# Optimization experiments

Hardware: AMD Instinct MI355X
Metric: run time of the kernel (lower is better)

## Reference

```python
import jax, jax.numpy as jnp
import numpy as np

ALPHA = 1.0          # gating temperature (train_alpha=False)
DEPTH = 4            # floor(log2(leaves=16))
LEAF_NUM = 16        # 2**DEPTH
N_INTERNAL = LEAF_NUM - 2  # nodes 1..14 (root handled separately)
B, D, OUT = 8192, 512, 64


def _prob(x, pw, aW, ab):
    # vectorized Node.prob with set_comps=True (comparators recomputed from batch mean)
    comp = -jnp.mean(x * pw, axis=0)                      # [in]
    dist = jax.nn.sigmoid(ALPHA * (pw * x + comp))        # [B, in]
    attn = jax.nn.softmax(x @ aW.T + ab, axis=-1)         # [B, in]
    return jnp.sum(dist * attn, axis=1, keepdims=True)    # [B, 1]


def setup_inputs() -> dict:
    key = jax.random.key(0)
    ks = jax.random.split(key, 12)
    s = 0.02
    return {
        "x": jax.random.normal(ks[0], (B, D), jnp.float32),
        # root node (input_size=D, output_size=D)
        "calc_W0": jax.random.normal(ks[1], (D, D), jnp.float32) * s,
        "calc_b0": jnp.zeros((D,), jnp.float32),
        "prob_w0": jax.random.uniform(ks[2], (D,), jnp.float32),
        "attn_W0": jax.random.normal(ks[3], (D, D), jnp.float32) * s,
        "attn_b0": jnp.zeros((D,), jnp.float32),
        # internal nodes 1..14 (input_size=2D, output_size=D), stacked
        "calc_W": jax.random.normal(ks[4], (N_INTERNAL, D, 2 * D), jnp.float32) * s,
        "calc_b": jnp.zeros((N_INTERNAL, D), jnp.float32),
        "prob_w": jax.random.uniform(ks[5], (N_INTERNAL, 2 * D), jnp.float32),
        "attn_W": jax.random.normal(ks[6], (N_INTERNAL, 2 * D, 2 * D), jnp.float32) * s,
        "attn_b": jnp.zeros((N_INTERNAL, 2 * D), jnp.float32),
        # leaf nodes: learned output vectors (torch.rand init)
        "leaf_out": jax.random.uniform(ks[7], (LEAF_NUM, OUT), jnp.float32),
    }


def reference(x, calc_W0, calc_b0, prob_w0, attn_W0, attn_b0,
              calc_W, calc_b, prob_w, attn_W, attn_b, leaf_out):
    outs, probab = {}, {}
    # root
    outs[0] = jax.nn.relu(x @ calc_W0.T + calc_b0)            # [B, D]
    p = _prob(x, prob_w0, attn_W0, attn_b0)                   # [B, 1]
    probab[1] = 1.0 - p
    probab[2] = p
    # internal nodes 1..leaf_num-2 (binary-tree routing)
    for n in range(1, LEAF_NUM - 1):
        parent = (n - 1) // 2
        inp = jnp.concatenate([outs[parent], x], axis=1)      # [B, 2D]
        outs[n] = jax.nn.relu(inp @ calc_W[n - 1].T + calc_b[n - 1])
        p = _prob(inp, prob_w[n - 1], attn_W[n - 1], attn_b[n - 1])
        probab[2 * n + 1] = probab[n] * (1.0 - p)
        probab[2 * n + 2] = probab[n] * p
    # leaves: indices LEAF_NUM-1 .. 2*LEAF_NUM-2
    leaf_p = jnp.concatenate([probab[i + LEAF_NUM - 1] for i in range(LEAF_NUM)], axis=1)  # [B, 16]
    # sum over leaves of probab * leaf_out == leaf_p @ leaf_out
    actions = leaf_p @ leaf_out                                # [B, OUT]
    return jax.nn.softmax(actions, axis=-1)
```

## Files before the change

kernel.cpp:

```cpp
#include <hip/hip_runtime.h>
#include <hip/hip_bf16.h>
#include <cstdint>


#define NROWS 8192
#define HALFD 512

typedef __bf16 bf16x8 __attribute__((ext_vector_type(8)));
typedef short  short8 __attribute__((ext_vector_type(8)));
typedef float  f32x4  __attribute__((ext_vector_type(4)));

union FragU { short8 s; bf16x8 b; };

struct GArgs {
  const __hip_bfloat16* A0[4];
  const __hip_bfloat16* Bw[4];
  const float* bias[4];
  const float* pw[4];
  const float* cm0[4];
  __hip_bfloat16* outB[4];
  float* csOut[4];
  float* S1[4];
  float* S2[4];
  int mode[4];
  int gx[4];
  int K[4];
};

__device__ __forceinline__ void gl2lds16(const void* g, void* l) {
  __builtin_amdgcn_global_load_lds((__attribute__((address_space(1))) void*)g,
                                   (__attribute__((address_space(3))) void*)l,
                                   16, 0, 0);
}

struct CvtArgs { const float* src[5]; __hip_bfloat16* dst[5]; int nblk[5]; };
__global__ void k_cvt(CvtArgs a) {
  int b = blockIdx.x, r = 0;
  while (b >= a.nblk[r]) { b -= a.nblk[r]; ++r; }
  const int i = (b * 256 + threadIdx.x) * 4;
  float4 v = *(const float4*)(a.src[r] + i);
  union { short4 s4; __hip_bfloat16 h[4]; } u;
  u.h[0] = __float2bfloat16(v.x);
  u.h[1] = __float2bfloat16(v.y);
  u.h[2] = __float2bfloat16(v.z);
  u.h[3] = __float2bfloat16(v.w);
  *(short4*)(a.dst[r] + i) = u.s4;
}

__global__ void k_colsum_f32(const float* __restrict__ src, float* __restrict__ dst) {
  int c  = blockIdx.x * 256 + threadIdx.x;
  int r0 = blockIdx.y * 256;
  float s = 0.f;
  for (int r = 0; r < 256; ++r) s += src[(size_t)(r0 + r) * HALFD + c];
  atomicAdd(&dst[c], s);
}

__global__ __launch_bounds__(256, 2)
void k_gemm(GArgs ga, const __hip_bfloat16* __restrict__ A1,
            const float* __restrict__ cm1) {
  __shared__ alignas(16) short As[128 * 64];
  __shared__ alignas(16) short Bs[128 * 64];

  const int z = blockIdx.z;
  const int id  = blockIdx.x + gridDim.x * blockIdx.y;
  const int xcd = id & 7;
  const int q   = id >> 3;
  const int bx  = q >> 3;
  const int by  = xcd * 8 + (q & 7);
  if (bx >= ga.gx[z]) return;

  const __hip_bfloat16* __restrict__ Ah0 = ga.A0[z];
  const __hip_bfloat16* __restrict__ Bw  = ga.Bw[z];
  const float* __restrict__ bias = ga.bias[z];
  const int K = ga.K[z];

  const int tid  = threadIdx.x;
  const int lane = tid & 63;
  const int wv   = tid >> 6;
  const int wm   = wv >> 1, wn = wv & 1;
  const int lr   = lane & 15, lg = lane >> 4;
  const int row0 = by * 128;
  const int col0 = bx * 128;

  f32x4 acc[4][4];
#pragma unroll
  for (int i = 0; i < 4; ++i)
#pragma unroll
    for (int j = 0; j < 4; ++j)
#pragma unroll
      for (int e = 0; e < 4; ++e) acc[i][j][e] = 0.f;

  const int sr = tid >> 3;
  const int sc = (((tid & 7) ^ (sr & 7)) << 3);
  const int sw = lr & 7;

  for (int kt = 0; kt < K; kt += 64) {
    const __hip_bfloat16* Asrc = (kt < HALFD) ? Ah0 : A1;
    const int kl = kt & (HALFD - 1);
    __syncthreads();
#pragma unroll
    for (int rnd = 0; rnd < 4; ++rnd) {
      const int r = rnd * 32 + sr;
      gl2lds16(Asrc + (size_t)(row0 + r) * HALFD + kl + sc,
               (char*)As + rnd * 4096 + wv * 1024);
      gl2lds16(Bw + (size_t)(col0 + r) * K + kt + sc,
               (char*)Bs + rnd * 4096 + wv * 1024);
    }
    __syncthreads();
#pragma unroll
    for (int kk = 0; kk < 64; kk += 32) {
      FragU a[4], b[4];
#pragma unroll
      for (int mi = 0; mi < 4; ++mi)
        a[mi].s = *(const short8*)(As + (wm * 64 + mi * 16 + lr) * 64 +
                                   ((((kk >> 3) + lg) ^ sw) << 3));
#pragma unroll
      for (int ni = 0; ni < 4; ++ni)
        b[ni].s = *(const short8*)(Bs + (wn * 64 + ni * 16 + lr) * 64 +
                                   ((((kk >> 3) + lg) ^ sw) << 3));
#pragma unroll
      for (int mi = 0; mi < 4; ++mi)
#pragma unroll
        for (int ni = 0; ni < 4; ++ni)
          acc[mi][ni] = __builtin_amdgcn_mfma_f32_16x16x32_bf16(a[mi].b, b[ni].b,
                                                               acc[mi][ni], 0, 0, 0);
    }
  }

  if (ga.mode[z] == 0) {
    __hip_bfloat16* outB = ga.outB[z];
    float* csOut = ga.csOut[z];
#pragma unroll
    for (int ni = 0; ni < 4; ++ni) {
      const int col  = col0 + wn * 64 + ni * 16 + lr;
      const float bv = bias[col];
      __hip_bfloat16* op = outB + (size_t)(col >> 9) * ((size_t)NROWS * HALFD) + (col & 511);
      float csum = 0.f;
#pragma unroll
      for (int mi = 0; mi < 4; ++mi) {
#pragma unroll
        for (int rg = 0; rg < 4; ++rg) {
          const int row = row0 + wm * 64 + mi * 16 + lg * 4 + rg;
          float v = acc[mi][ni][rg] + bv;
          v = v > 0.f ? v : 0.f;
          csum += v;
          op[(size_t)row * HALFD] = __float2bfloat16(v);
        }
      }
      csum += __shfl_xor(csum, 16);
      csum += __shfl_xor(csum, 32);
      if (lg == 0) atomicAdd(&csOut[col], csum);
    }
  } else {
    const float* __restrict__ pw  = ga.pw[z];
    const float* __restrict__ cm0 = ga.cm0[z];
    const int node  = col0 >> 10;
    const int slice = ((bx & 7) << 1) | wn;
    float* s1p = ga.S1[z] + (size_t)(node * 16 + slice) * NROWS;
    float* s2p = ga.S2[z] + (size_t)(node * 16 + slice) * NROWS;
    float bv[4], pwv[4], cmv[4];
    const __hip_bfloat16* Ain[4];
#pragma unroll
    for (int ni = 0; ni < 4; ++ni) {
      const int col = col0 + wn * 64 + ni * 16 + lr;
      bv[ni]  = bias[col];
      pwv[ni] = pw[col];
      const int ii   = col & 1023;
      const int half = ii >> 9;
      const int cc   = ii & 511;
      cmv[ni] = (half ? cm1[cc] : cm0[cc]) * (1.f / 8192.f);
      Ain[ni] = (half ? A1 : Ah0) + cc;
    }
#pragma unroll
    for (int mi = 0; mi < 4; ++mi) {
#pragma unroll
      for (int rg = 0; rg < 4; ++rg) {
        const int row = row0 + wm * 64 + mi * 16 + lg * 4 + rg;
        float s1 = 0.f, s2 = 0.f;
#pragma unroll
        for (int ni = 0; ni < 4; ++ni) {
          const float l = acc[mi][ni][rg] + bv[ni];
          const float e = __expf(l);
          const float inpv = __bfloat162float(Ain[ni][(size_t)row * HALFD]);
          const float zz = pwv[ni] * (inpv - cmv[ni]);
          const float dist = 1.f / (1.f + __expf(-zz));
          s1 += e;
          s2 += dist * e;
        }
#pragma unroll
        for (int off = 1; off < 16; off <<= 1) {
          s1 += __shfl_xor(s1, off);
          s2 += __shfl_xor(s2, off);
        }
        if (lr == 0) {
          s1p[row] = s1;
          s2p[row] = s2;
        }
      }
    }
  }
}

__global__ void k_finalize(const float* __restrict__ S1, const float* __restrict__ S2,
                           const float* __restrict__ leaf_out, float* __restrict__ out) {
  const int r    = (blockIdx.x * 256 + threadIdx.x) >> 6;
  const int lane = threadIdx.x & 63;
  float pb[31];
  pb[0] = 1.f;
#pragma unroll
  for (int n = 0; n < 15; ++n) {
    float a1 = 0.f, a2 = 0.f;
#pragma unroll
    for (int s = 0; s < 16; ++s) {
      a1 += S1[((size_t)n * 16 + s) * NROWS + r];
      a2 += S2[((size_t)n * 16 + s) * NROWS + r];
    }
    const float p = a2 / a1;
    pb[2 * n + 1] = pb[n] * (1.f - p);
    pb[2 * n + 2] = pb[n] * p;
  }
  float a = 0.f;
#pragma unroll
  for (int i = 0; i < 16; ++i) a += pb[15 + i] * leaf_out[i * 64 + lane];
  float m = a;
#pragma unroll
  for (int off = 1; off < 64; off <<= 1) m = fmaxf(m, __shfl_xor(m, off));
  const float e = __expf(a - m);
  float s = e;
#pragma unroll
  for (int off = 1; off < 64; off <<= 1) s += __shfl_xor(s, off);
  out[(size_t)r * 64 + lane] = e / s;
}

static constexpr size_t O_S1   = 0;
static constexpr size_t O_S2   = O_S1 + (size_t)15 * 16 * NROWS * 4;
static constexpr size_t O_XSUM = O_S2 + (size_t)15 * 16 * NROWS * 4;
static constexpr size_t O_CS   = O_XSUM + 512 * 4;
static constexpr size_t O_ZEND = O_CS + 7 * 512 * 4;
static constexpr size_t O_XB   = O_ZEND;
static constexpr size_t O_OUTS = O_XB + (size_t)NROWS * HALFD * 2;
static constexpr size_t O_CW0  = O_OUTS + 7 * (size_t)NROWS * HALFD * 2;
static constexpr size_t O_AW0  = O_CW0 + (size_t)512 * 512 * 2;
static constexpr size_t O_CW   = O_AW0 + (size_t)512 * 512 * 2;
static constexpr size_t O_AW   = O_CW + (size_t)14 * 512 * 1024 * 2;

extern "C" void kernel_launch(void* const* d_in, const int* in_sizes, int n_in,
                              void* d_out, int out_size, void* d_ws, size_t ws_size,
                              hipStream_t stream) {
  const float* x        = (const float*)d_in[0];
  const float* calc_b0  = (const float*)d_in[2];
  const float* prob_w0  = (const float*)d_in[3];
  const float* attn_b0  = (const float*)d_in[5];
  const float* calc_b   = (const float*)d_in[7];
  const float* prob_w   = (const float*)d_in[8];
  const float* attn_b   = (const float*)d_in[10];
  const float* leaf_out = (const float*)d_in[11];
  float* out = (float*)d_out;
  char* ws = (char*)d_ws;

  float* S1   = (float*)(ws + O_S1);
  float* S2   = (float*)(ws + O_S2);
  float* xsum = (float*)(ws + O_XSUM);
  float* cs   = (float*)(ws + O_CS);
  __hip_bfloat16* xb   = (__hip_bfloat16*)(ws + O_XB);
  __hip_bfloat16* outs = (__hip_bfloat16*)(ws + O_OUTS);
  __hip_bfloat16* cW0b = (__hip_bfloat16*)(ws + O_CW0);
  __hip_bfloat16* aW0b = (__hip_bfloat16*)(ws + O_AW0);
  __hip_bfloat16* cWb  = (__hip_bfloat16*)(ws + O_CW);
  __hip_bfloat16* aWb  = (__hip_bfloat16*)(ws + O_AW);
  const size_t OSZ = (size_t)NROWS * HALFD;
  const size_t NSL = (size_t)16 * NROWS;

  hipMemsetAsync(d_ws, 0, O_ZEND, stream);

  {
    CvtArgs ca{};
    ca.src[0] = x;                     ca.dst[0] = xb;   ca.nblk[0] = NROWS * HALFD / 1024;
    ca.src[1] = (const float*)d_in[1]; ca.dst[1] = cW0b; ca.nblk[1] = 512 * 512 / 1024;
    ca.src[2] = (const float*)d_in[4]; ca.dst[2] = aW0b; ca.nblk[2] = 512 * 512 / 1024;
    ca.src[3] = (const float*)d_in[6]; ca.dst[3] = cWb;  ca.nblk[3] = 14 * 512 * 1024 / 1024;
    ca.src[4] = (const float*)d_in[9]; ca.dst[4] = aWb;  ca.nblk[4] = 14 * 1024 * 1024 / 1024;
    int tot = ca.nblk[0] + ca.nblk[1] + ca.nblk[2] + ca.nblk[3] + ca.nblk[4];
    k_cvt<<<tot, 256, 0, stream>>>(ca);
  }
  k_colsum_f32<<<dim3(2, 32), 256, 0, stream>>>(x, xsum);

  {
    GArgs ga{};
    ga.mode[0] = 0; ga.gx[0] = 4; ga.K[0] = 512;
    ga.A0[0] = xb; ga.Bw[0] = cW0b; ga.bias[0] = calc_b0;
    ga.outB[0] = outs; ga.csOut[0] = cs;
    ga.mode[1] = 1; ga.gx[1] = 4; ga.K[1] = 512;
    ga.A0[1] = xb; ga.Bw[1] = aW0b; ga.bias[1] = attn_b0;
    ga.pw[1] = prob_w0; ga.cm0[1] = xsum;
    ga.S1[1] = S1; ga.S2[1] = S2;
    k_gemm<<<dim3(4, 64, 2), 256, 0, stream>>>(ga, xb, xsum);
  }
  {
    GArgs ga{};
    ga.mode[0] = 0; ga.gx[0] = 8; ga.K[0] = 1024;
    ga.A0[0] = outs; ga.Bw[0] = cWb; ga.bias[0] = calc_b;
    ga.outB[0] = outs + OSZ; ga.csOut[0] = cs + 512;
    ga.mode[1] = 1; ga.gx[1] = 16; ga.K[1] = 1024;
    ga.A0[1] = outs; ga.Bw[1] = aWb; ga.bias[1] = attn_b;
    ga.pw[1] = prob_w; ga.cm0[1] = cs;
    ga.S1[1] = S1 + (size_t)1 * NSL; ga.S2[1] = S2 + (size_t)1 * NSL;
    k_gemm<<<dim3(16, 64, 2), 256, 0, stream>>>(ga, xb, xsum);
  }
  {
    GArgs ga{};
    for (int i = 0; i < 2; ++i) {
      ga.mode[i] = 0; ga.gx[i] = 8; ga.K[i] = 1024;
      ga.A0[i] = outs + (size_t)(1 + i) * OSZ;
      ga.Bw[i] = cWb + (size_t)(2 + 2 * i) * 512 * 1024;
      ga.bias[i] = calc_b + (2 + 2 * i) * 512;
      ga.outB[i] = outs + (size_t)(3 + 2 * i) * OSZ;
      ga.csOut[i] = cs + (size_t)(3 + 2 * i) * 512;
    }
    for (int i = 0; i < 2; ++i) {
      const int zi = 2 + i;
      ga.mode[zi] = 1; ga.gx[zi] = 16; ga.K[zi] = 1024;
      ga.A0[zi] = outs + (size_t)(1 + i) * OSZ;
      ga.Bw[zi] = aWb + (size_t)(2 + 2 * i) * 1024 * 1024;
      ga.bias[zi] = attn_b + (2 + 2 * i) * 1024;
      ga.pw[zi] = prob_w + (2 + 2 * i) * 1024;
      ga.cm0[zi] = cs + (size_t)(1 + i) * 512;
      ga.S1[zi] = S1 + (size_t)(3 + 2 * i) * NSL;
      ga.S2[zi] = S2 + (size_t)(3 + 2 * i) * NSL;
    }
    k_gemm<<<dim3(16, 64, 4), 256, 0, stream>>>(ga, xb, xsum);
  }
  {
    GArgs ga{};
    for (int i = 0; i < 4; ++i) {
      ga.mode[i] = 1; ga.gx[i] = 16; ga.K[i] = 1024;
      ga.A0[i] = outs + (size_t)(3 + i) * OSZ;
      ga.Bw[i] = aWb + (size_t)(6 + 2 * i) * 1024 * 1024;
      ga.bias[i] = attn_b + (6 + 2 * i) * 1024;
      ga.pw[i] = prob_w + (6 + 2 * i) * 1024;
      ga.cm0[i] = cs + (size_t)(3 + i) * 512;
      ga.S1[i] = S1 + (size_t)(7 + 2 * i) * NSL;
      ga.S2[i] = S2 + (size_t)(7 + 2 * i) * NSL;
    }
    k_gemm<<<dim3(16, 64, 4), 256, 0, stream>>>(ga, xb, xsum);
  }

  k_finalize<<<NROWS * 64 / 256, 256, 0, stream>>>(S1, S2, leaf_out, out);
}
```

Baseline: 636.2 us.

## Use 256x256 GEMM tiles with 512 threads and double-buffered LDS prefetch

The GEMM kernel moves from 128x128 tiles with 4 waves to 256x256 tiles with 8 waves, and each wave now covers 128x64 outputs with twice the accumulators. LDS is double-buffered so the next K slab is loaded while the current one is multiplied, leaving one barrier per iteration instead of two. This aims to raise data reuse per byte loaded and hide global-to-LDS latency. In exchange it uses 128KB of LDS per block and more registers, which may cut occupancy, and the grid shrinks to fewer, larger blocks, which may leave CUs idle.

Measured after the change: 668.8 us. +5.1%, slower.

```diff
diff --git a/kernel.cpp b/kernel.cpp
--- a/kernel.cpp
+++ b/kernel.cpp
@@ -55,18 +55,18 @@
   atomicAdd(&dst[c], s);
 }
 
-__global__ __launch_bounds__(256, 2)
+__global__ __launch_bounds__(512, 2)
 void k_gemm(GArgs ga, const __hip_bfloat16* __restrict__ A1,
             const float* __restrict__ cm1) {
-  __shared__ alignas(16) short As[128 * 64];
-  __shared__ alignas(16) short Bs[128 * 64];
+  __shared__ alignas(16) short As[2][256 * 64];
+  __shared__ alignas(16) short Bs[2][256 * 64];
 
   const int z = blockIdx.z;
   const int id  = blockIdx.x + gridDim.x * blockIdx.y;
   const int xcd = id & 7;
   const int q   = id >> 3;
-  const int bx  = q >> 3;
-  const int by  = xcd * 8 + (q & 7);
+  const int bx  = q >> 2;
+  const int by  = xcd * 4 + (q & 3);
   if (bx >= ga.gx[z]) return;
 
   const __hip_bfloat16* __restrict__ Ah0 = ga.A0[z];
@@ -77,54 +77,69 @@
   const int tid  = threadIdx.x;
   const int lane = tid & 63;
   const int wv   = tid >> 6;
-  const int wm   = wv >> 1, wn = wv & 1;
+  const int wm   = wv >> 2, wn = wv & 3;
   const int lr   = lane & 15, lg = lane >> 4;
-  const int row0 = by * 128;
-  const int col0 = bx * 128;
-
-  f32x4 acc[4][4];
-#pragma unroll
-  for (int i = 0; i < 4; ++i)
+  const int sw   = lr & 7;
+  const int row0 = by * 256;
+  const int col0 = bx * 256;
+
+  f32x4 acc[8][4];
+#pragma unroll
+  for (int i = 0; i < 8; ++i)
 #pragma unroll
     for (int j = 0; j < 4; ++j)
 #pragma unroll
       for (int e = 0; e < 4; ++e) acc[i][j][e] = 0.f;
 
-  const int sr = tid >> 3;
-  const int sc = (((tid & 7) ^ (sr & 7)) << 3);
-  const int sw = lr & 7;
-
+  const int sr  = tid >> 3;
+  const int sc  = (((tid & 7) ^ (sr & 7)) << 3);
+  const int wvB = wv * 1024;
+
+#pragma unroll
+  for (int rnd = 0; rnd < 4; ++rnd) {
+    const int r = rnd * 64 + sr;
+    gl2lds16(Ah0 + (size_t)(row0 + r) * HALFD + sc, (char*)As[0] + rnd * 8192 + wvB);
+    gl2lds16(Bw  + (size_t)(col0 + r) * K + sc,     (char*)Bs[0] + rnd * 8192 + wvB);
+  }
+  __syncthreads();
+
+  int cur = 0;
   for (int kt = 0; kt < K; kt += 64) {
-    const __hip_bfloat16* Asrc = (kt < HALFD) ? Ah0 : A1;
-    const int kl = kt & (HALFD - 1);
-    __syncthreads();
-#pragma unroll
-    for (int rnd = 0; rnd < 4; ++rnd) {
-      const int r = rnd * 32 + sr;
-      gl2lds16(Asrc + (size_t)(row0 + r) * HALFD + kl + sc,
-               (char*)As + rnd * 4096 + wv * 1024);
-      gl2lds16(Bw + (size_t)(col0 + r) * K + kt + sc,
-               (char*)Bs + rnd * 4096 + wv * 1024);
-    }
-    __syncthreads();
+    const int kn = kt + 64;
+    if (kn < K) {
+      const __hip_bfloat16* Asrc = (kn < HALFD) ? Ah0 : A1;
+      const int kl = kn & (HALFD - 1);
+#pragma unroll
+      for (int rnd = 0; rnd < 4; ++rnd) {
+        const int r = rnd * 64 + sr;
+        gl2lds16(Asrc + (size_t)(row0 + r) * HALFD + kl + sc,
+                 (char*)As[cur ^ 1] + rnd * 8192 + wvB);
+        gl2lds16(Bw + (size_t)(col0 + r) * K + kn + sc,
+                 (char*)Bs[cur ^ 1] + rnd * 8192 + wvB);
+      }
+    }
+    const short* Ab = As[cur];
+    const short* Bb = Bs[cur];
 #pragma unroll
     for (int kk = 0; kk < 64; kk += 32) {
-      FragU a[4], b[4];
-#pragma unroll
-      for (int mi = 0; mi < 4; ++mi)
-        a[mi].s = *(const short8*)(As + (wm * 64 + mi * 16 + lr) * 64 +
+      FragU a[8], b[4];
+#pragma unroll
+      for (int mi = 0; mi < 8; ++mi)
+        a[mi].s = *(const short8*)(Ab + (wm * 128 + mi * 16 + lr) * 64 +
                                    ((((kk >> 3) + lg) ^ sw) << 3));
 #pragma unroll
       for (int ni = 0; ni < 4; ++ni)
-        b[ni].s = *(const short8*)(Bs + (wn * 64 + ni * 16 + lr) * 64 +
+        b[ni].s = *(const short8*)(Bb + (wn * 64 + ni * 16 + lr) * 64 +
                                    ((((kk >> 3) + lg) ^ sw) << 3));
 #pragma unroll
-      for (int mi = 0; mi < 4; ++mi)
+      for (int mi = 0; mi < 8; ++mi)
 #pragma unroll
         for (int ni = 0; ni < 4; ++ni)
           acc[mi][ni] = __builtin_amdgcn_mfma_f32_16x16x32_bf16(a[mi].b, b[ni].b,
                                                                acc[mi][ni], 0, 0, 0);
     }
+    __syncthreads();
+    cur ^= 1;
   }
 
   if (ga.mode[z] == 0) {
@@ -137,10 +152,10 @@
       __hip_bfloat16* op = outB + (size_t)(col >> 9) * ((size_t)NROWS * HALFD) + (col & 511);
       float csum = 0.f;
 #pragma unroll
-      for (int mi = 0; mi < 4; ++mi) {
+      for (int mi = 0; mi < 8; ++mi) {
 #pragma unroll
         for (int rg = 0; rg < 4; ++rg) {
-          const int row = row0 + wm * 64 + mi * 16 + lg * 4 + rg;
+          const int row = row0 + wm * 128 + mi * 16 + lg * 4 + rg;
           float v = acc[mi][ni][rg] + bv;
           v = v > 0.f ? v : 0.f;
           csum += v;
@@ -155,7 +170,7 @@
     const float* __restrict__ pw  = ga.pw[z];
     const float* __restrict__ cm0 = ga.cm0[z];
     const int node  = col0 >> 10;
-    const int slice = ((bx & 7) << 1) | wn;
+    const int slice = ((bx & 3) << 2) | wn;
     float* s1p = ga.S1[z] + (size_t)(node * 16 + slice) * NROWS;
     float* s2p = ga.S2[z] + (size_t)(node * 16 + slice) * NROWS;
     float bv[4], pwv[4], cmv[4];
@@ -172,10 +187,10 @@
       Ain[ni] = (half ? A1 : Ah0) + cc;
     }
 #pragma unroll
-    for (int mi = 0; mi < 4; ++mi) {
+    for (int mi = 0; mi < 8; ++mi) {
 #pragma unroll
       for (int rg = 0; rg < 4; ++rg) {
-        const int row = row0 + wm * 64 + mi * 16 + lg * 4 + rg;
+        const int row = row0 + wm * 128 + mi * 16 + lg * 4 + rg;
         float s1 = 0.f, s2 = 0.f;
 #pragma unroll
         for (int ni = 0; ni < 4; ++ni) {
@@ -287,30 +302,30 @@
 
   {
     GArgs ga{};
-    ga.mode[0] = 0; ga.gx[0] = 4; ga.K[0] = 512;
+    ga.mode[0] = 0; ga.gx[0] = 2; ga.K[0] = 512;
     ga.A0[0] = xb; ga.Bw[0] = cW0b; ga.bias[0] = calc_b0;
     ga.outB[0] = outs; ga.csOut[0] = cs;
-    ga.mode[1] = 1; ga.gx[1] = 4; ga.K[1] = 512;
+    ga.mode[1] = 1; ga.gx[1] = 2; ga.K[1] = 512;
     ga.A0[1] = xb; ga.Bw[1] = aW0b; ga.bias[1] = attn_b0;
     ga.pw[1] = prob_w0; ga.cm0[1] = xsum;
     ga.S1[1] = S1; ga.S2[1] = S2;
-    k_gemm<<<dim3(4, 64, 2), 256, 0, stream>>>(ga, xb, xsum);
+    k_gemm<<<dim3(2, 32, 2), 512, 0, stream>>>(ga, xb, xsum);
   }
   {
     GArgs ga{};
-    ga.mode[0] = 0; ga.gx[0] = 8; ga.K[0] = 1024;
+    ga.mode[0] = 0; ga.gx[0] = 4; ga.K[0] = 1024;
     ga.A0[0] = outs; ga.Bw[0] = cWb; ga.bias[0] = calc_b;
     ga.outB[0] = outs + OSZ; ga.csOut[0] = cs + 512;
-    ga.mode[1] = 1; ga.gx[1] = 16; ga.K[1] = 1024;
+    ga.mode[1] = 1; ga.gx[1] = 8; ga.K[1] = 1024;
     ga.A0[1] = outs; ga.Bw[1] = aWb; ga.bias[1] = attn_b;
     ga.pw[1] = prob_w; ga.cm0[1] = cs;
     ga.S1[1] = S1 + (size_t)1 * NSL; ga.S2[1] = S2 + (size_t)1 * NSL;
-    k_gemm<<<dim3(16, 64, 2), 256, 0, stream>>>(ga, xb, xsum);
+    k_gemm<<<dim3(8, 32, 2), 512, 0, stream>>>(ga, xb, xsum);
   }
   {
     GArgs ga{};
     for (int i = 0; i < 2; ++i) {
-      ga.mode[i] = 0; ga.gx[i] = 8; ga.K[i] = 1024;
+      ga.mode[i] = 0; ga.gx[i] = 4; ga.K[i] = 1024;
       ga.A0[i] = outs + (size_t)(1 + i) * OSZ;
       ga.Bw[i] = cWb + (size_t)(2 + 2 * i) * 512 * 1024;
       ga.bias[i] = calc_b + (2 + 2 * i) * 512;
@@ -319,7 +334,7 @@
     }
     for (int i = 0; i < 2; ++i) {
       const int zi = 2 + i;
-      ga.mode[zi] = 1; ga.gx[zi] = 16; ga.K[zi] = 1024;
+      ga.mode[zi] = 1; ga.gx[zi] = 8; ga.K[zi] = 1024;
       ga.A0[zi] = outs + (size_t)(1 + i) * OSZ;
       ga.Bw[zi] = aWb + (size_t)(2 + 2 * i) * 1024 * 1024;
       ga.bias[zi] = attn_b + (2 + 2 * i) * 1024;
@@ -328,12 +343,12 @@
       ga.S1[zi] = S1 + (size_t)(3 + 2 * i) * NSL;
       ga.S2[zi] = S2 + (size_t)(3 + 2 * i) * NSL;
     }
-    k_gemm<<<dim3(16, 64, 4), 256, 0, stream>>>(ga, xb, xsum);
+    k_gemm<<<dim3(8, 32, 4), 512, 0, stream>>>(ga, xb, xsum);
   }
   {
     GArgs ga{};
     for (int i = 0; i < 4; ++i) {
-      ga.mode[i] = 1; ga.gx[i] = 16; ga.K[i] = 1024;
+      ga.mode[i] = 1; ga.gx[i] = 8; ga.K[i] = 1024;
       ga.A0[i] = outs + (size_t)(3 + i) * OSZ;
       ga.Bw[i] = aWb + (size_t)(6 + 2 * i) * 1024 * 1024;
       ga.bias[i] = attn_b + (6 + 2 * i) * 1024;
@@ -342,7 +357,7 @@
       ga.S1[i] = S1 + (size_t)(7 + 2 * i) * NSL;
       ga.S2[i] = S2 + (size_t)(7 + 2 * i) * NSL;
     }
-    k_gemm<<<dim3(16, 64, 4), 256, 0, stream>>>(ga, xb, xsum);
+    k_gemm<<<dim3(8, 32, 4), 512, 0, stream>>>(ga, xb, xsum);
   }
 
   k_finalize<<<NROWS * 64 / 256, 256, 0, stream>>>(S1, S2, leaf_out, out);
```
